# Performance work log

Measured on AMD Instinct MI355X. Metric: run time of the kernel, lower is better.

Reference implementation:

```python
import jax, jax.numpy as jnp
import numpy as np

BS, SEQ, D, H = 2, 2048, 1024, 16
HD = D // H  # head_dim = 64


def setup_inputs() -> dict:
    key = jax.random.key(0)
    kx, kw = jax.random.split(key)
    x = jax.random.normal(kx, (BS, SEQ, D), dtype=jnp.float32)
    # qkv Linear: weight [3D, D] (xavier_normal), bias zeros
    std = float(np.sqrt(2.0 / (D + 3 * D)))
    W_qkv = jax.random.normal(kw, (3 * D, D), dtype=jnp.float32) * std
    b_qkv = jnp.zeros((3 * D,), dtype=jnp.float32)
    return {"x": x, "W_qkv": W_qkv, "b_qkv": b_qkv}


def reference(x, W_qkv, b_qkv):
    bs, seq_len, embed_dim = x.shape
    # fused QKV projection: [bs, seq, 3D]
    qkv = x @ W_qkv.T + b_qkv
    qkv = qkv.reshape(bs, seq_len, 3, H, HD)
    qkv = jnp.transpose(qkv, (2, 0, 3, 1, 4))  # [3, bs, H, seq, HD]
    Q, K, V = qkv[0], qkv[1], qkv[2]
    # past_kv is None -> total_len == seq_len, past_len == 0
    scores = jnp.einsum("bhqd,bhkd->bhqk", Q, K) / jnp.sqrt(jnp.float32(HD))
    # causal mask: True above diagonal -> -inf
    mask = jnp.triu(jnp.ones((seq_len, seq_len), dtype=bool), k=1)
    scores = jnp.where(mask[None, None, :, :], -jnp.inf, scores)
    probs = jax.nn.softmax(scores, axis=-1)
    # attn_dropout = 0.0 (eval) -> identity
    out = jnp.einsum("bhqk,bhkd->bhqd", probs, V)
    out = jnp.transpose(out, (0, 2, 1, 3)).reshape(bs, seq_len, embed_dim)
    return (out, (K, V))
```

## Files before the change

kernel.cpp:

```cpp
#include <hip/hip_runtime.h>

typedef __bf16 bf16_t;
typedef __bf16 bf16x8 __attribute__((ext_vector_type(8)));
typedef float f32x4 __attribute__((ext_vector_type(4)));
typedef unsigned long long u64;

__device__ __forceinline__ unsigned short bfbits(float f) {
  unsigned u = __float_as_uint(f);
  u += 0x7fffu + ((u >> 16) & 1u);
  return (unsigned short)(u >> 16);
}
__device__ __forceinline__ bf16_t f2bf(float f) {
  unsigned short s = bfbits(f);
  union { unsigned short s; bf16_t b; } cv; cv.s = s; return cv.b;
}

__device__ __forceinline__ void gl16(const void* g, void* l) {
  __builtin_amdgcn_global_load_lds(
      (const __attribute__((address_space(1))) void*)g,
      (__attribute__((address_space(3))) void*)l,
      16, 0, 0);
}

__global__ __launch_bounds__(256) void cvt_kernel(const float* __restrict__ x,
                                                  const float* __restrict__ Wf,
                                                  bf16_t* __restrict__ xb,
                                                  bf16_t* __restrict__ wb) {
  const int i = blockIdx.x * 256 + threadIdx.x;
  const float* src; bf16_t* dst; int j;
  if (i < 524288) { j = i; src = x; dst = xb; }
  else            { j = i - 524288; src = Wf; dst = wb; }
  const float4* s = (const float4*)src + (size_t)j * 2;
  float4 a = s[0], b = s[1];
  bf16x8 o;
  o[0] = f2bf(a.x); o[1] = f2bf(a.y); o[2] = f2bf(a.z); o[3] = f2bf(a.w);
  o[4] = f2bf(b.x); o[5] = f2bf(b.y); o[6] = f2bf(b.z); o[7] = f2bf(b.w);
  const int row = j >> 7, jr = j & 127;
  const int dstc = (row << 7) + (jr & ~3) + ((jr & 3) ^ ((row >> 1) & 3));
  *((bf16x8*)dst + dstc) = o;
}

#define GEMM_K 1024
__global__ __launch_bounds__(256) void qkv_gemm(
    const bf16_t* __restrict__ A,
    const bf16_t* __restrict__ B,
    const float* __restrict__ bias,
    float* __restrict__ Ko, float* __restrict__ Vo,
    bf16_t* __restrict__ Qb, bf16_t* __restrict__ Kb,
    bf16_t* __restrict__ Vt,
    int* __restrict__ qcnt)
{
  if (blockIdx.x == 0 && threadIdx.x == 0) *qcnt = 0;
  __shared__ bf16_t lsA[3][4096];
  __shared__ bf16_t lsB[3][4096];
  const int tid = threadIdx.x;
  const int lane = tid & 63;
  const int ln = lane & 15, qd = lane >> 4;
  const int wid = tid >> 6;
  const int wm = wid & 1, wn = wid >> 1;
  const int xcd = blockIdx.x & 7;
  const int j = blockIdx.x >> 3;
  const int bn = xcd * 3 + (j % 3);
  const int bm = j / 3;
  const int m0 = bm * 128, n0 = bn * 128;
  const int qs = qd ^ ((ln >> 1) & 3);

  f32x4 acc[4][4] = {};

  const int c0 = tid, c1 = tid + 256;
  const bf16_t* ga0 = A + (size_t)(m0 + (c0 >> 2)) * GEMM_K + (c0 & 3) * 8;
  const bf16_t* ga1 = A + (size_t)(m0 + (c1 >> 2)) * GEMM_K + (c1 & 3) * 8;
  const bf16_t* gb0 = B + (size_t)(n0 + (c0 >> 2)) * GEMM_K + (c0 & 3) * 8;
  const bf16_t* gb1 = B + (size_t)(n0 + (c1 >> 2)) * GEMM_K + (c1 & 3) * 8;

  auto stage = [&](int t, int slot) {
    const int ko = t * 32;
    gl16(ga0 + ko, &lsA[slot][c0 * 8]);
    gl16(ga1 + ko, &lsA[slot][c1 * 8]);
    gl16(gb0 + ko, &lsB[slot][c0 * 8]);
    gl16(gb1 + ko, &lsB[slot][c1 * 8]);
  };
  auto compute = [&](int slot) {
    bf16x8 af[4], bf[4];
#pragma unroll
    for (int mi = 0; mi < 4; ++mi)
      af[mi] = *(const bf16x8*)&lsA[slot][(wm * 64 + mi * 16 + ln) * 32 + qs * 8];
#pragma unroll
    for (int ni = 0; ni < 4; ++ni)
      bf[ni] = *(const bf16x8*)&lsB[slot][(wn * 64 + ni * 16 + ln) * 32 + qs * 8];
#pragma unroll
    for (int mi = 0; mi < 4; ++mi)
#pragma unroll
      for (int ni = 0; ni < 4; ++ni)
        acc[mi][ni] = __builtin_amdgcn_mfma_f32_16x16x32_bf16(af[mi], bf[ni], acc[mi][ni], 0, 0, 0);
  };

  stage(0, 0);
  stage(1, 1);
  int cur = 0, nxt = 2;
  for (int t = 0; t < 30; ++t) {
    asm volatile("s_waitcnt vmcnt(4)" ::: "memory");
    __builtin_amdgcn_s_barrier();
    stage(t + 2, nxt);
    compute(cur);
    cur = (cur == 2) ? 0 : cur + 1;
    nxt = (nxt == 2) ? 0 : nxt + 1;
  }
  asm volatile("s_waitcnt vmcnt(4)" ::: "memory");
  __builtin_amdgcn_s_barrier();
  compute(cur);
  cur = (cur == 2) ? 0 : cur + 1;
  asm volatile("s_waitcnt vmcnt(0)" ::: "memory");
  __builtin_amdgcn_s_barrier();
  compute(cur);

  const int sec = n0 >> 10;
#pragma unroll
  for (int mi = 0; mi < 4; ++mi) {
#pragma unroll
    for (int ni = 0; ni < 4; ++ni) {
      const int colg = n0 + wn * 64 + ni * 16 + ln;
      const float bv = bias[colg];
      const int cc = colg & 1023, h = cc >> 6, hd = cc & 63;
      if (sec == 2) {
        unsigned u[4];
#pragma unroll
        for (int r = 0; r < 4; ++r) {
          const int mg = m0 + wm * 64 + mi * 16 + qd * 4 + r;
          const int b = mg >> 11, s = mg & 2047;
          const float val = acc[mi][ni][r] + bv;
          Vo[((size_t)((b * 16 + h) * 2048 + s)) * 64 + hd] = val;
          u[r] = __float_as_uint(val);
        }
        const int mg0 = m0 + wm * 64 + mi * 16 + qd * 4;
        const int b0 = mg0 >> 11, s0 = mg0 & 2047;
        const unsigned lo = (u[1] & 0xFFFF0000u) | (u[0] >> 16);
        const unsigned hi = (u[3] & 0xFFFF0000u) | (u[2] >> 16);
        const size_t vb = (size_t)(b0 * 16 + h) * 131072 + (size_t)(s0 >> 6) * 4096 +
                          (size_t)hd * 64 + ((((s0 >> 3) & 7) ^ (hd & 7)) << 3) + (s0 & 7);
        *(u64*)&Vt[vb] = ((u64)hi << 32) | lo;
      } else {
#pragma unroll
        for (int r = 0; r < 4; ++r) {
          const int mg = m0 + wm * 64 + mi * 16 + qd * 4 + r;
          const int b = mg >> 11, s = mg & 2047;
          const float val = acc[mi][ni][r] + bv;
          const int bhi = b * 16 + h;
          const size_t sidx = (size_t)bhi * 131072 + (size_t)(s >> 6) * 4096 +
                              (size_t)(s & 63) * 64 + (((hd >> 3) ^ (s & 7)) << 3) + (hd & 7);
          if (sec == 0) {
            Qb[sidx] = f2bf(val * 0.18033688f);
          } else {
            Ko[((size_t)(bhi * 2048 + s)) * 64 + hd] = val;
            Kb[sidx] = f2bf(val);
          }
        }
      }
    }
  }
}

__global__ __launch_bounds__(256) void attn_kernel(
    const bf16_t* __restrict__ Qb,
    const bf16_t* __restrict__ Kb,
    const bf16_t* __restrict__ Vt,
    float* __restrict__ Out,
    int* __restrict__ qcnt)
{
  __shared__ bf16_t lq[8192];
  __shared__ bf16_t lk[8192];
  __shared__ bf16_t lv[8192];
  __shared__ bf16_t lp[8192];
  __shared__ int task_sh;
  const int tid = threadIdx.x;
  const int lane = tid & 63, ln = lane & 15, qd = lane >> 4;
  const int w = tid >> 6;
  const int l7 = ln & 7;

  for (;;) {
    __syncthreads();
    if (tid == 0) task_sh = atomicAdd(qcnt, 1);
    __syncthreads();
    const int task = task_sh;
    if (task >= 512) break;
    const int it = (task < 256) ? (15 - (task >> 5)) : ((task - 256) >> 5);
    const int bh = task & 31;
    const int b = bh >> 4, h = bh & 15;

    const bf16_t* qbase = Qb + (size_t)bh * 131072 + (size_t)it * 8192;
    const bf16_t* kbase = Kb + (size_t)bh * 131072;
    const bf16_t* vbase = Vt + (size_t)bh * 131072;

#pragma unroll
    for (int i = 0; i < 4; ++i) {
      const int cc = tid + i * 256;
      gl16(qbase + cc * 8, &lq[cc * 8]);
      gl16(kbase + cc * 8, &lk[cc * 8]);
      gl16(vbase + cc * 8, &lv[cc * 8]);
    }
    __syncthreads();

    bf16x8 afq[2][2];
#pragma unroll
    for (int kk = 0; kk < 2; ++kk)
#pragma unroll
      for (int qi = 0; qi < 2; ++qi) {
        const int row = w * 32 + qi * 16 + ln;
        afq[kk][qi] = *(const bf16x8*)&lq[(row >> 6) * 4096 + (row & 63) * 64 +
                                          (((kk * 4 + qd) ^ l7) << 3)];
      }

    f32x4 oc[2][4] = {};
    float lsum[2] = {0.f, 0.f};
    const int qg = it * 128 + w * 32 + ln;

    for (int st = 0; st <= it; ++st) {
      if (st > 0) {
        __syncthreads();
#pragma unroll
        for (int i = 0; i < 4; ++i) {
          const int cc = tid + i * 256;
          gl16(kbase + (size_t)st * 8192 + cc * 8, &lk[cc * 8]);
          gl16(vbase + (size_t)st * 8192 + cc * 8, &lv[cc * 8]);
        }
        __syncthreads();
      }
      const bool diag = (st == it);

#pragma unroll
      for (int h2 = 0; h2 < 2; ++h2) {
        const int lofs = h2 * 4096;
        f32x4 sa[4][2] = {};
#pragma unroll
        for (int kk = 0; kk < 2; ++kk) {
          bf16x8 ak[4];
#pragma unroll
          for (int ki = 0; ki < 4; ++ki)
            ak[ki] = *(const bf16x8*)&lk[lofs + (ki * 16 + ln) * 64 + (((kk * 4 + qd) ^ l7) << 3)];
#pragma unroll
          for (int ki = 0; ki < 4; ++ki)
#pragma unroll
            for (int qi = 0; qi < 2; ++qi)
              sa[ki][qi] = __builtin_amdgcn_mfma_f32_16x16x32_bf16(ak[ki], afq[kk][qi], sa[ki][qi], 0, 0, 0);
        }

#pragma unroll
        for (int qi = 0; qi < 2; ++qi) {
          const int qgl = qg + qi * 16;
          const int q = w * 32 + qi * 16 + ln;
#pragma unroll
          for (int ki = 0; ki < 4; ++ki) {
            const int kb0 = (st * 2 + h2) * 64 + ki * 16 + qd * 4;
            float p0 = __builtin_amdgcn_exp2f(sa[ki][qi][0]);
            float p1 = __builtin_amdgcn_exp2f(sa[ki][qi][1]);
            float p2 = __builtin_amdgcn_exp2f(sa[ki][qi][2]);
            float p3 = __builtin_amdgcn_exp2f(sa[ki][qi][3]);
            if (diag) {
              if (kb0 + 0 > qgl) p0 = 0.f;
              if (kb0 + 1 > qgl) p1 = 0.f;
              if (kb0 + 2 > qgl) p2 = 0.f;
              if (kb0 + 3 > qgl) p3 = 0.f;
            }
            lsum[qi] += (p0 + p1) + (p2 + p3);
            const unsigned lo = (__float_as_uint(p1) & 0xFFFF0000u) | (__float_as_uint(p0) >> 16);
            const unsigned hi = (__float_as_uint(p3) & 0xFFFF0000u) | (__float_as_uint(p2) >> 16);
            const int g = (ki * 2 + (qd >> 1)) ^ l7;
            *(u64*)&lp[q * 64 + g * 8 + (qd & 1) * 4] = ((u64)hi << 32) | lo;
          }
        }

#pragma unroll
        for (int kk = 0; kk < 2; ++kk) {
          bf16x8 afp[2], bfv[4];
#pragma unroll
          for (int qi = 0; qi < 2; ++qi) {
            const int q = w * 32 + qi * 16 + ln;
            afp[qi] = *(const bf16x8*)&lp[q * 64 + (((kk * 4 + qd) ^ l7) << 3)];
          }
#pragma unroll
          for (int ni = 0; ni < 4; ++ni)
            bfv[ni] = *(const bf16x8*)&lv[lofs + (ni * 16 + ln) * 64 + (((kk * 4 + qd) ^ l7) << 3)];
#pragma unroll
          for (int qi = 0; qi < 2; ++qi)
#pragma unroll
            for (int ni = 0; ni < 4; ++ni)
              oc[qi][ni] = __builtin_amdgcn_mfma_f32_16x16x32_bf16(afp[qi], bfv[ni], oc[qi][ni], 0, 0, 0);
        }
      }
    }

    float lsq[2];
#pragma unroll
    for (int qi = 0; qi < 2; ++qi) {
      float ls = lsum[qi];
      ls += __shfl_xor(ls, 16);
      ls += __shfl_xor(ls, 32);
      lsq[qi] = ls;
    }
#pragma unroll
    for (int qi = 0; qi < 2; ++qi) {
#pragma unroll
      for (int r = 0; r < 4; ++r) {
        const float lval = __shfl(lsq[qi], qd * 4 + r);
        const float inv = 1.0f / lval;
        const int rowq = it * 128 + w * 32 + qi * 16 + qd * 4 + r;
#pragma unroll
        for (int ni = 0; ni < 4; ++ni) {
          const int colh = ni * 16 + ln;
          Out[(size_t)(b * 2048 + rowq) * 1024 + h * 64 + colh] = oc[qi][ni][r] * inv;
        }
      }
    }
  }
}

extern "C" void kernel_launch(void* const* d_in, const int* in_sizes, int n_in,
                              void* d_out, int out_size, void* d_ws, size_t ws_size,
                              hipStream_t stream) {
  const float* x = (const float*)d_in[0];
  const float* W = (const float*)d_in[1];
  const float* bq = (const float*)d_in[2];
  float* out = (float*)d_out;
  float* Ko = out + 4194304;
  float* Vo = out + 8388608;
  char* ws = (char*)d_ws;
  bf16_t* xb = (bf16_t*)ws;
  bf16_t* wb = (bf16_t*)(ws + 8388608);
  bf16_t* Qb = (bf16_t*)(ws + 14680064);
  bf16_t* Kb = (bf16_t*)(ws + 23068672);
  bf16_t* Vt = (bf16_t*)(ws + 31457280);
  int*    qcnt = (int*)(ws + 39845888);

  hipLaunchKernelGGL(cvt_kernel, dim3(3584), dim3(256), 0, stream, x, W, xb, wb);
  hipLaunchKernelGGL(qkv_gemm, dim3(768), dim3(256), 0, stream, xb, wb, bq, Ko, Vo, Qb, Kb, Vt, qcnt);
  hipLaunchKernelGGL(attn_kernel, dim3(512), dim3(256), 0, stream, Qb, Kb, Vt, out, qcnt);
}
```

Before: 172.5 us.

## Double-buffer K/V tiles in LDS and prefetch the next tile during compute

```diff
diff --git a/kernel.cpp b/kernel.cpp
--- a/kernel.cpp
+++ b/kernel.cpp
@@ -168,8 +168,8 @@
     int* __restrict__ qcnt)
 {
   __shared__ bf16_t lq[8192];
-  __shared__ bf16_t lk[8192];
-  __shared__ bf16_t lv[8192];
+  __shared__ bf16_t lk[2][4096];
+  __shared__ bf16_t lv[2][4096];
   __shared__ bf16_t lp[8192];
   __shared__ int task_sh;
   const int tid = threadIdx.x;
@@ -191,14 +191,24 @@
     const bf16_t* kbase = Kb + (size_t)bh * 131072;
     const bf16_t* vbase = Vt + (size_t)bh * 131072;
 
+    auto stageKV = [&](int t, int slot) {
+      const size_t off = (size_t)t * 4096;
+#pragma unroll
+      for (int i = 0; i < 2; ++i) {
+        const int cc = tid + i * 256;
+        gl16(kbase + off + cc * 8, &lk[slot][cc * 8]);
+        gl16(vbase + off + cc * 8, &lv[slot][cc * 8]);
+      }
+    };
+
 #pragma unroll
     for (int i = 0; i < 4; ++i) {
       const int cc = tid + i * 256;
       gl16(qbase + cc * 8, &lq[cc * 8]);
-      gl16(kbase + cc * 8, &lk[cc * 8]);
-      gl16(vbase + cc * 8, &lv[cc * 8]);
-    }
-    __syncthreads();
+    }
+    stageKV(0, 0);
+    asm volatile("s_waitcnt vmcnt(0)" ::: "memory");
+    __builtin_amdgcn_s_barrier();
 
     bf16x8 afq[2][2];
 #pragma unroll
@@ -213,80 +223,77 @@
     f32x4 oc[2][4] = {};
     float lsum[2] = {0.f, 0.f};
     const int qg = it * 128 + w * 32 + ln;
-
-    for (int st = 0; st <= it; ++st) {
-      if (st > 0) {
-        __syncthreads();
-#pragma unroll
-        for (int i = 0; i < 4; ++i) {
-          const int cc = tid + i * 256;
-          gl16(kbase + (size_t)st * 8192 + cc * 8, &lk[cc * 8]);
-          gl16(vbase + (size_t)st * 8192 + cc * 8, &lv[cc * 8]);
-        }
-        __syncthreads();
-      }
-      const bool diag = (st == it);
-
-#pragma unroll
-      for (int h2 = 0; h2 < 2; ++h2) {
-        const int lofs = h2 * 4096;
-        f32x4 sa[4][2] = {};
-#pragma unroll
-        for (int kk = 0; kk < 2; ++kk) {
-          bf16x8 ak[4];
-#pragma unroll
-          for (int ki = 0; ki < 4; ++ki)
-            ak[ki] = *(const bf16x8*)&lk[lofs + (ki * 16 + ln) * 64 + (((kk * 4 + qd) ^ l7) << 3)];
-#pragma unroll
-          for (int ki = 0; ki < 4; ++ki)
-#pragma unroll
-            for (int qi = 0; qi < 2; ++qi)
-              sa[ki][qi] = __builtin_amdgcn_mfma_f32_16x16x32_bf16(ak[ki], afq[kk][qi], sa[ki][qi], 0, 0, 0);
-        }
-
+    const int nt = 2 * (it + 1);
+    int cur = 0;
+
+    for (int t = 0; t < nt; ++t) {
+      if (t + 1 < nt) stageKV(t + 1, cur ^ 1);
+      const bool diag = (t >= 2 * it);
+
+      f32x4 sa[4][2] = {};
+      __builtin_amdgcn_s_setprio(1);
+#pragma unroll
+      for (int kk = 0; kk < 2; ++kk) {
+        bf16x8 ak[4];
+#pragma unroll
+        for (int ki = 0; ki < 4; ++ki)
+          ak[ki] = *(const bf16x8*)&lk[cur][(ki * 16 + ln) * 64 + (((kk * 4 + qd) ^ l7) << 3)];
+#pragma unroll
+        for (int ki = 0; ki < 4; ++ki)
+#pragma unroll
+          for (int qi = 0; qi < 2; ++qi)
+            sa[ki][qi] = __builtin_amdgcn_mfma_f32_16x16x32_bf16(ak[ki], afq[kk][qi], sa[ki][qi], 0, 0, 0);
+      }
+      __builtin_amdgcn_s_setprio(0);
+
+#pragma unroll
+      for (int qi = 0; qi < 2; ++qi) {
+        const int qgl = qg + qi * 16;
+        const int q = w * 32 + qi * 16 + ln;
+#pragma unroll
+        for (int ki = 0; ki < 4; ++ki) {
+          const int kb0 = t * 64 + ki * 16 + qd * 4;
+          float p0 = __builtin_amdgcn_exp2f(sa[ki][qi][0]);
+          float p1 = __builtin_amdgcn_exp2f(sa[ki][qi][1]);
+          float p2 = __builtin_amdgcn_exp2f(sa[ki][qi][2]);
+          float p3 = __builtin_amdgcn_exp2f(sa[ki][qi][3]);
+          if (diag) {
+            if (kb0 + 0 > qgl) p0 = 0.f;
+            if (kb0 + 1 > qgl) p1 = 0.f;
+            if (kb0 + 2 > qgl) p2 = 0.f;
+            if (kb0 + 3 > qgl) p3 = 0.f;
+          }
+          lsum[qi] += (p0 + p1) + (p2 + p3);
+          const unsigned lo = (__float_as_uint(p1) & 0xFFFF0000u) | (__float_as_uint(p0) >> 16);
+          const unsigned hi = (__float_as_uint(p3) & 0xFFFF0000u) | (__float_as_uint(p2) >> 16);
+          const int g = (ki * 2 + (qd >> 1)) ^ l7;
+          *(u64*)&lp[q * 64 + g * 8 + (qd & 1) * 4] = ((u64)hi << 32) | lo;
+        }
+      }
+
+      __builtin_amdgcn_s_setprio(1);
+#pragma unroll
+      for (int kk = 0; kk < 2; ++kk) {
+        bf16x8 afp[2], bfv[4];
 #pragma unroll
         for (int qi = 0; qi < 2; ++qi) {
-          const int qgl = qg + qi * 16;
           const int q = w * 32 + qi * 16 + ln;
-#pragma unroll
-          for (int ki = 0; ki < 4; ++ki) {
-            const int kb0 = (st * 2 + h2) * 64 + ki * 16 + qd * 4;
-            float p0 = __builtin_amdgcn_exp2f(sa[ki][qi][0]);
-            float p1 = __builtin_amdgcn_exp2f(sa[ki][qi][1]);
-            float p2 = __builtin_amdgcn_exp2f(sa[ki][qi][2]);
-            float p3 = __builtin_amdgcn_exp2f(sa[ki][qi][3]);
-            if (diag) {
-              if (kb0 + 0 > qgl) p0 = 0.f;
-              if (kb0 + 1 > qgl) p1 = 0.f;
-              if (kb0 + 2 > qgl) p2 = 0.f;
-              if (kb0 + 3 > qgl) p3 = 0.f;
-            }
-            lsum[qi] += (p0 + p1) + (p2 + p3);
-            const unsigned lo = (__float_as_uint(p1) & 0xFFFF0000u) | (__float_as_uint(p0) >> 16);
-            const unsigned hi = (__float_as_uint(p3) & 0xFFFF0000u) | (__float_as_uint(p2) >> 16);
-            const int g = (ki * 2 + (qd >> 1)) ^ l7;
-            *(u64*)&lp[q * 64 + g * 8 + (qd & 1) * 4] = ((u64)hi << 32) | lo;
-          }
-        }
-
-#pragma unroll
-        for (int kk = 0; kk < 2; ++kk) {
-          bf16x8 afp[2], bfv[4];
-#pragma unroll
-          for (int qi = 0; qi < 2; ++qi) {
-            const int q = w * 32 + qi * 16 + ln;
-            afp[qi] = *(const bf16x8*)&lp[q * 64 + (((kk * 4 + qd) ^ l7) << 3)];
-          }
+          afp[qi] = *(const bf16x8*)&lp[q * 64 + (((kk * 4 + qd) ^ l7) << 3)];
+        }
+#pragma unroll
+        for (int ni = 0; ni < 4; ++ni)
+          bfv[ni] = *(const bf16x8*)&lv[cur][(ni * 16 + ln) * 64 + (((kk * 4 + qd) ^ l7) << 3)];
+#pragma unroll
+        for (int qi = 0; qi < 2; ++qi)
 #pragma unroll
           for (int ni = 0; ni < 4; ++ni)
-            bfv[ni] = *(const bf16x8*)&lv[lofs + (ni * 16 + ln) * 64 + (((kk * 4 + qd) ^ l7) << 3)];
-#pragma unroll
-          for (int qi = 0; qi < 2; ++qi)
-#pragma unroll
-            for (int ni = 0; ni < 4; ++ni)
-              oc[qi][ni] = __builtin_amdgcn_mfma_f32_16x16x32_bf16(afp[qi], bfv[ni], oc[qi][ni], 0, 0, 0);
-        }
-      }
+            oc[qi][ni] = __builtin_amdgcn_mfma_f32_16x16x32_bf16(afp[qi], bfv[ni], oc[qi][ni], 0, 0, 0);
+      }
+      __builtin_amdgcn_s_setprio(0);
+
+      asm volatile("s_waitcnt vmcnt(0)" ::: "memory");
+      __builtin_amdgcn_s_barrier();
+      cur ^= 1;
     }
 
     float lsq[2];
```

Result: slower. 181.7 us (+5.3%).
